# Performance work log

Measured on AMD Instinct MI355X. Metric: run time of the kernel, lower is better.

Reference implementation:

```python
import jax, jax.numpy as jnp
import numpy as np

L = 6        # num_coupling_layers
T_DIM = 64   # t_dim
HALF = T_DIM // 2
COND = 128   # cond_dim
HID = 1024   # hidden_dim
B = 32768


def setup_inputs() -> dict:
    key = jax.random.key(0)
    ks = jax.random.split(key, 8)
    s_in = 1.0 / np.sqrt(HALF + COND)
    s_h = 1.0 / np.sqrt(HID)
    T = jax.random.normal(ks[0], (B, T_DIM), dtype=jnp.float32)
    cond = jax.random.normal(ks[1], (B, COND), dtype=jnp.float32)
    W1 = jax.random.normal(ks[2], (L, HALF + COND, HID), dtype=jnp.float32) * s_in
    b1 = jnp.zeros((L, HID), dtype=jnp.float32)
    W2 = jax.random.normal(ks[3], (L, HID, HID), dtype=jnp.float32) * s_h
    b2 = jnp.zeros((L, HID), dtype=jnp.float32)
    W3 = jax.random.normal(ks[4], (L, HID, 2 * HALF), dtype=jnp.float32) * s_h
    b3 = jnp.zeros((L, 2 * HALF), dtype=jnp.float32)
    return {"T": T, "cond": cond, "W1": W1, "b1": b1, "W2": W2, "b2": b2, "W3": W3, "b3": b3}


def reference(T, cond, W1, b1, W2, b2, W3, b3):
    # Conditional normalizing flow: 6 affine coupling layers with alternating
    # contiguous half masks. Even layers transform the first half, odd the second.
    def mlp(h, i):
        x = jax.nn.relu(h @ W1[i] + b1[i])
        x = jax.nn.relu(x @ W2[i] + b2[i])
        return x @ W3[i] + b3[i]

    z = T
    log_det = jnp.zeros(T.shape[0], dtype=T.dtype)
    for i in range(L):
        if i % 2 == 0:
            masked, unmasked = z[:, :HALF], z[:, HALF:]
        else:
            masked, unmasked = z[:, HALF:], z[:, :HALF]
        params = mlp(jnp.concatenate([unmasked, cond], axis=1), i)
        s = jnp.tanh(params[:, :HALF])
        t_shift = params[:, HALF:]
        y_masked = masked * jnp.exp(s) + t_shift
        if i % 2 == 0:
            z = jnp.concatenate([y_masked, unmasked], axis=1)
        else:
            z = jnp.concatenate([unmasked, y_masked], axis=1)
        log_det = log_det + jnp.sum(s, axis=1)
    return z, log_det
```

## Files before the change

### kernel.cpp

```cpp
#include <hip/hip_runtime.h>
#include <hip/hip_fp16.h>
#include <stdint.h>

typedef _Float16 f16;
typedef _Float16 f16x8 __attribute__((ext_vector_type(8)));
typedef float f32x4 __attribute__((ext_vector_type(4)));

#define NB 32768
#define LAYERS 6
#define AK 160
#define HID 1024

__device__ __forceinline__ void async_copy16(const void* g, void* l) {
  __builtin_amdgcn_global_load_lds(
      (const __attribute__((address_space(1))) void*)g,
      (__attribute__((address_space(3))) void*)l, 16, 0, 0);
}

__device__ __forceinline__ void wtrans_tile(const float* __restrict__ W,
                                            f16* __restrict__ Wt,
                                            const int K_, const int N_,
                                            const int bx, const int by,
                                            const int bz, float (*t)[65])
{
  const long off = (long)bz * K_ * N_;
  const float* Wl = W + off;
  f16* Wtl = Wt + off;
  const int k0 = by * 64, n0 = bx * 64;
  const int tx = threadIdx.x & 63, ty4 = threadIdx.x >> 6;
#pragma unroll
  for (int r = ty4; r < 64; r += 4) {
    const int k = k0 + r;
    if (k < K_) t[r][tx] = Wl[(long)k * N_ + n0 + tx];
  }
  __syncthreads();
  const int k = k0 + tx;
  if (k < K_) {
#pragma unroll
    for (int r = ty4; r < 64; r += 4) {
      const int n = n0 + r;
      Wtl[(long)n * K_ + k] = (f16)t[tx][r];
    }
  }
}

__global__ void prep_all(const float* __restrict__ T, const float* __restrict__ cond,
                         const float* __restrict__ W1, const float* __restrict__ W2,
                         const float* __restrict__ W3,
                         float* __restrict__ z, float* __restrict__ ld,
                         f16* __restrict__ A,
                         f16* __restrict__ W1t, f16* __restrict__ W2t,
                         f16* __restrict__ W3t)
{
  __shared__ float t[64][65];
  const int b = blockIdx.x;
  if (b < 2048) {
    const int S1 = NB * 64;
    const int S2 = S1 + NB;
    const int S3 = S2 + NB * 32;
    const int S4 = S3 + NB * 128;
    for (int i = b * blockDim.x + threadIdx.x; i < S4; i += 2048 * blockDim.x) {
      if (i < S1) {
        z[i] = T[i];
      } else if (i < S2) {
        ld[i - S1] = 0.0f;
      } else if (i < S3) {
        int r = i - S2;
        int row = r >> 5, j = r & 31;
        A[(size_t)row * AK + j] = (f16)T[row * 64 + 32 + j];
      } else {
        int r = i - S3;
        int row = r >> 7, j = r & 127;
        A[(size_t)row * AK + 32 + j] = (f16)cond[r];
      }
    }
  } else if (b < 2048 + 288) {
    const int l = b - 2048;
    wtrans_tile(W1, W1t, AK, 1024, l % 16, (l / 16) % 3, l / 48, t);
  } else if (b < 2048 + 288 + 1536) {
    const int l = b - (2048 + 288);
    wtrans_tile(W2, W2t, HID, 1024, l % 16, (l / 16) % 16, l / 256, t);
  } else {
    const int l = b - (2048 + 288 + 1536);
    wtrans_tile(W3, W3t, HID, 64, 0, l % 16, l / 16, t);
  }
}

__global__ __launch_bounds__(256, 2)
void gemm1_full(const f16* __restrict__ A,
                const f16* __restrict__ Wt,
                const float* __restrict__ bias,
                f16* __restrict__ C)
{
  __shared__ __align__(16) f16 As[128 * 160];
  __shared__ __align__(16) f16 Bs[128 * 160];
  const int tid  = threadIdx.x;
  const int lane = tid & 63;
  const int wave = tid >> 6;
  const int c15  = lane & 15;
  const int quad = lane >> 4;
  const int wm = (wave & 1) * 64;
  const int wn = (wave >> 1) * 64;

  const int b = blockIdx.x;
  const int x = b & 7, i = b >> 3;
  const long rowStart = (long)(x * 32 + (i >> 3)) * 128;
  const long colStart = (long)(i & 7) * 128;

  const f16* Ab = A  + rowStart * AK;
  const f16* Bb = Wt + colStart * AK;

#pragma unroll
  for (int it = 0; it < 10; ++it) {
    const int f = it * 256 + tid;
    const int row = f / 20;
    const int ch  = f - row * 20;
    const int chs = ch ^ ((row >> 1) & 3);
    async_copy16(Ab + (long)row * AK + chs * 8, &As[0] + (long)f * 8);
    async_copy16(Bb + (long)row * AK + chs * 8, &Bs[0] + (long)f * 8);
  }
  __syncthreads();

  f32x4 acc[4][4] = {};
#pragma unroll
  for (int kt = 0; kt < 5; ++kt) {
    f16x8 a[4], bf[4];
#pragma unroll
    for (int mi = 0; mi < 4; ++mi) {
      const int R = wm + mi * 16 + c15;
      a[mi] = *(const f16x8*)&As[(R * 20 + kt * 4 + (quad ^ ((R >> 1) & 3))) * 8];
    }
#pragma unroll
    for (int ni = 0; ni < 4; ++ni) {
      const int R = wn + ni * 16 + c15;
      bf[ni] = *(const f16x8*)&Bs[(R * 20 + kt * 4 + (quad ^ ((R >> 1) & 3))) * 8];
    }
#pragma unroll
    for (int mi = 0; mi < 4; ++mi)
#pragma unroll
      for (int ni = 0; ni < 4; ++ni)
        acc[mi][ni] = __builtin_amdgcn_mfma_f32_16x16x32_f16(
            a[mi], bf[ni], acc[mi][ni], 0, 0, 0);
  }

#pragma unroll
  for (int ni = 0; ni < 4; ++ni) {
    const long gn = colStart + wn + ni * 16 + c15;
    const float bv = bias[gn];
#pragma unroll
    for (int mi = 0; mi < 4; ++mi) {
#pragma unroll
      for (int r = 0; r < 4; ++r) {
        const long gm = rowStart + wm + mi * 16 + quad * 4 + r;
        float v = acc[mi][ni][r] + bv;
        v = fmaxf(v, 0.0f);
        C[gm * HID + gn] = (f16)v;
      }
    }
  }
}

#define RD_A(dst, base, mq) \
  _Pragma("unroll") \
  for (int mi = 0; mi < 4; ++mi) { \
    const int r_ = wm + (mq) * 64 + mi * 16 + c15; \
    _Pragma("unroll") \
    for (int ks = 0; ks < 2; ++ks) \
      dst[mi][ks] = *(const f16x8*)&(base)[r_ * 64 + ((((ks << 2) + quad) ^ (r_ & 7)) << 3)]; \
  }
#define RD_B(dst, base, nq) \
  _Pragma("unroll") \
  for (int ni = 0; ni < 2; ++ni) { \
    const int r_ = wn + (nq) * 32 + ni * 16 + c15; \
    _Pragma("unroll") \
    for (int ks = 0; ks < 2; ++ks) \
      dst[ni][ks] = *(const f16x8*)&(base)[r_ * 64 + ((((ks << 2) + quad) ^ (r_ & 7)) << 3)]; \
  }
#define MM(am, an, afr, bfr) \
  __builtin_amdgcn_s_setprio(1); \
  _Pragma("unroll") \
  for (int ks = 0; ks < 2; ++ks) \
  _Pragma("unroll") \
  for (int mi = 0; mi < 4; ++mi) \
  _Pragma("unroll") \
  for (int ni = 0; ni < 2; ++ni) \
    acc[(am) + mi][(an) + ni] = __builtin_amdgcn_mfma_f32_16x16x32_f16( \
        afr[mi][ks], bfr[ni][ks], acc[(am) + mi][(an) + ni], 0, 0, 0); \
  __builtin_amdgcn_s_setprio(0);
#define BARRIER __builtin_amdgcn_s_barrier()
#define LGKM0   asm volatile("s_waitcnt lgkmcnt(0)")

__global__ __launch_bounds__(512, 2)
void gemm2_8p(const f16* __restrict__ A,
              const f16* __restrict__ Wt,
              const float* __restrict__ bias,
              f16* __restrict__ C)
{
  __shared__ __align__(16) f16 As[2][16384];
  __shared__ __align__(16) f16 Bs[2][16384];

  const int tid  = threadIdx.x;
  const int lane = tid & 63;
  const int wave = tid >> 6;
  const int c15  = lane & 15;
  const int quad = lane >> 4;
  const int wm = (wave >> 2) * 128;
  const int wn = (wave & 3) * 64;

  const int b = blockIdx.x;
  const int wgid = (b & 7) * 64 + (b >> 3);
  const long rowStart = (long)(wgid >> 2) * 256;
  const long colStart = (long)(wgid & 3) * 256;

  const f16* Ab = A  + rowStart * HID;
  const f16* Bb = Wt + colStart * HID;

  const int rh0 = tid >> 3;
  const int ch0 = tid & 7;
  const long g0 = (long)rh0 * HID + ((ch0 ^ (rh0 & 7)) << 3);
  const long g1 = (long)(64 + rh0) * HID + ((ch0 ^ ((64 + rh0) & 7)) << 3);
  const int l0 = tid << 3;
  const int l1 = (512 + tid) << 3;

  auto stA = [&](int kt, int h) {
    const f16* src = Ab + (long)h * 128 * HID + (long)kt * 64;
    f16* dst = &As[kt & 1][h * 8192];
    async_copy16(src + g0, dst + l0);
    async_copy16(src + g1, dst + l1);
  };
  auto stB = [&](int kt, int h) {
    const f16* src = Bb + (long)h * 128 * HID + (long)kt * 64;
    f16* dst = &Bs[kt & 1][h * 8192];
    async_copy16(src + g0, dst + l0);
    async_copy16(src + g1, dst + l1);
  };

  stB(0, 0); stA(0, 0); stB(0, 1); stA(0, 1);
  stB(1, 0); stA(1, 0);
  asm volatile("s_waitcnt vmcnt(4)");
  BARRIER;

  f32x4 acc[8][4] = {};

#pragma unroll 1
  for (int t = 0; t < 8; ++t) {
    const int kt0 = 2 * t, kt1 = 2 * t + 1;
    const f16* asx = &As[0][0];
    const f16* bsx = &Bs[0][0];
    const f16* asy = &As[1][0];
    const f16* bsy = &Bs[1][0];
    const bool pre = (t < 7);
    f16x8 a0[4][2], a1[4][2], b0[2][2], b1[2][2];

    RD_A(a0, asx, 0);
    RD_B(b0, bsx, 0);
    stB(kt1, 1);
    BARRIER; LGKM0;
    MM(0, 0, a0, b0);
    BARRIER;

    RD_B(b1, bsx, 1);
    stA(kt1, 1);
    BARRIER; LGKM0;
    MM(0, 2, a0, b1);
    BARRIER;

    RD_A(a1, asx, 1);
    if (pre) stB(kt0 + 2, 0);
    BARRIER; LGKM0;
    MM(4, 0, a1, b0);
    BARRIER;

    if (pre) stA(kt0 + 2, 0);
    MM(4, 2, a1, b1);
    if (pre) { asm volatile("s_waitcnt vmcnt(4)"); }
    else     { asm volatile("s_waitcnt vmcnt(0)"); }
    BARRIER;

    RD_A(a0, asy, 0);
    RD_B(b0, bsy, 0);
    if (pre) stB(kt0 + 2, 1);
    BARRIER; LGKM0;
    MM(0, 0, a0, b0);
    BARRIER;

    RD_B(b1, bsy, 1);
    if (pre) stA(kt0 + 2, 1);
    BARRIER; LGKM0;
    MM(0, 2, a0, b1);
    BARRIER;

    RD_A(a1, asy, 1);
    if (pre) stB(kt1 + 2, 0);
    BARRIER; LGKM0;
    MM(4, 0, a1, b0);
    BARRIER;

    if (pre) stA(kt1 + 2, 0);
    MM(4, 2, a1, b1);
    if (pre) { asm volatile("s_waitcnt vmcnt(4)"); }
    else     { asm volatile("s_waitcnt vmcnt(0)"); }
    BARRIER;
  }

#pragma unroll
  for (int nii = 0; nii < 4; ++nii) {
    const int nof = (nii >> 1) * 32 + (nii & 1) * 16;
    const long gn = colStart + wn + nof + c15;
    const float bv = bias[gn];
#pragma unroll
    for (int mii = 0; mii < 8; ++mii) {
      const int mof = (mii >> 2) * 64 + (mii & 3) * 16;
#pragma unroll
      for (int r = 0; r < 4; ++r) {
        const long gm = rowStart + wm + mof + quad * 4 + r;
        float v = acc[mii][nii][r] + bv;
        C[gm * HID + gn] = (f16)fmaxf(v, 0.0f);
      }
    }
  }
}

__global__ __launch_bounds__(256, 2)
void gemm3_coupling(const f16* __restrict__ X2, const f16* __restrict__ W3t,
                    const float* __restrict__ b3, float* __restrict__ z,
                    float* __restrict__ log_det, f16* __restrict__ Anext,
                    const int maskoff)
{
  __shared__ __align__(16) f16 As[2][64 * 64];
  __shared__ __align__(16) f16 Bs[2][64 * 64];
  const int tid = threadIdx.x;
  const int wave = tid >> 6, lane = tid & 63;
  const int c15 = lane & 15, quad = lane >> 4;
  const int wm = wave * 16;
  const long rowStart = (long)blockIdx.x * 64;

  const f16* Ab = X2 + rowStart * HID;
  const int brow = tid >> 3;
  const int bkc  = ((tid & 7) ^ (brow & 7)) * 8;

  f32x4 acc[4] = {};

  auto stage = [&](int c, int sel) {
    const long kb = (long)c * 64;
#pragma unroll
    for (int q = 0; q < 2; ++q) {
      async_copy16(Ab  + (long)(q * 32 + brow) * HID + kb + bkc,
                   &As[sel][0] + (q * 256 + wave * 64) * 8);
      async_copy16(W3t + (long)(q * 32 + brow) * HID + kb + bkc,
                   &Bs[sel][0] + (q * 256 + wave * 64) * 8);
    }
  };

  stage(0, 0);
  for (int c = 0; c < 16; ++c) {
    __syncthreads();
    if (c + 1 < 16) stage(c + 1, (c + 1) & 1);
    const f16* as = &As[c & 1][0];
    const f16* bs = &Bs[c & 1][0];

#pragma unroll
    for (int s = 0; s < 2; ++s) {
      const int Ra = wm + c15;
      f16x8 a = *(const f16x8*)&as[(Ra * 8 + ((s * 4 + quad) ^ (Ra & 7))) * 8];
      f16x8 bf[4];
#pragma unroll
      for (int ni = 0; ni < 4; ++ni) {
        const int R = ni * 16 + c15;
        bf[ni] = *(const f16x8*)&bs[(R * 8 + ((s * 4 + quad) ^ (R & 7))) * 8];
      }
#pragma unroll
      for (int ni = 0; ni < 4; ++ni)
        acc[ni] = __builtin_amdgcn_mfma_f32_16x16x32_f16(a, bf[ni], acc[ni], 0, 0, 0);
    }
  }

  float sp[4] = {0.0f, 0.0f, 0.0f, 0.0f};
#pragma unroll
  for (int ni = 0; ni < 2; ++ni) {
    const int j = ni * 16 + c15;
    const float bs = b3[j];
    const float bt = b3[32 + j];
#pragma unroll
    for (int r = 0; r < 4; ++r) {
      const long gm = rowStart + wm + quad * 4 + r;
      const float sv = acc[ni][r] + bs;
      const float e2 = __expf(2.0f * sv);
      const float s  = 1.0f - 2.0f / (e2 + 1.0f);
      const float tv = acc[ni + 2][r] + bt;
      const float m  = z[gm * 64 + maskoff + j];
      const float y  = fmaf(m, __expf(s), tv);
      z[gm * 64 + maskoff + j] = y;
      Anext[gm * AK + j] = (f16)y;
      sp[r] += s;
    }
  }
#pragma unroll
  for (int r = 0; r < 4; ++r) {
    float v = sp[r];
    v += __shfl_xor(v, 1);
    v += __shfl_xor(v, 2);
    v += __shfl_xor(v, 4);
    v += __shfl_xor(v, 8);
    if (c15 == 0) {
      const long gm = rowStart + wm + quad * 4 + r;
      log_det[gm] += v;
    }
  }
}

extern "C" void kernel_launch(void* const* d_in, const int* in_sizes, int n_in,
                              void* d_out, int out_size, void* d_ws, size_t ws_size,
                              hipStream_t stream) {
  (void)in_sizes; (void)n_in; (void)out_size; (void)ws_size;
  const float* T    = (const float*)d_in[0];
  const float* cond = (const float*)d_in[1];
  const float* W1   = (const float*)d_in[2];
  const float* b1   = (const float*)d_in[3];
  const float* W2   = (const float*)d_in[4];
  const float* b2   = (const float*)d_in[5];
  const float* W3   = (const float*)d_in[6];
  const float* b3   = (const float*)d_in[7];

  float* z  = (float*)d_out;
  float* ld = z + (size_t)NB * 64;

  f16* A   = (f16*)d_ws;
  f16* X1  = A   + (size_t)NB * AK;
  f16* X2  = X1  + (size_t)NB * HID;
  f16* W1t = X2  + (size_t)NB * HID;
  f16* W2t = W1t + (size_t)6 * 1024 * 160;
  f16* W3t = W2t + ((size_t)6 << 20);

  prep_all<<<3968, 256, 0, stream>>>(T, cond, W1, W2, W3,
                                     z, ld, A, W1t, W2t, W3t);

  const int g1 = (NB / 128) * (HID / 128);
  const int g2 = (NB / 256) * (HID / 256);
  for (int l = 0; l < LAYERS; ++l) {
    gemm1_full<<<g1, 256, 0, stream>>>(A, W1t + (size_t)l * 1024 * AK,
                                       b1 + l * 1024, X1);
    gemm2_8p<<<g2, 512, 0, stream>>>(X1, W2t + ((size_t)l << 20),
                                     b2 + l * 1024, X2);
    const int maskoff = (l & 1) ? 32 : 0;
    gemm3_coupling<<<NB / 64, 256, 0, stream>>>(X2, W3t + (size_t)l * 64 * 1024,
                                                b3 + l * 64, z, ld, A, maskoff);
  }
}
```

Before: 826.7 us.

## Reschedule gemm2 main loop with register-rotated fragments and partial LDS waits

Rewrites the 1024x1024 hidden GEMM's inner loop so LDS fragment reads for the next MFMA block are issued before the current block runs. It rotates two register fragment sets and waits with partial lgkmcnt counts instead of draining to zero. Global-to-LDS prefetch now loads a whole k-tile up front, issued in pairs per phase, with sched_barrier fencing around vmcnt waits. The aim is to hide LDS latency behind MFMA work, at the cost of more live registers and fragile wait-count correctness.

```diff
diff --git a/kernel.cpp b/kernel.cpp
--- a/kernel.cpp
+++ b/kernel.cpp
@@ -188,10 +188,11 @@
         afr[mi][ks], bfr[ni][ks], acc[(am) + mi][(an) + ni], 0, 0, 0); \
   __builtin_amdgcn_s_setprio(0);
 #define BARRIER __builtin_amdgcn_s_barrier()
-#define LGKM0   asm volatile("s_waitcnt lgkmcnt(0)")
+#define SCHED0  __builtin_amdgcn_sched_barrier(0)
+#define LGKM(n) asm volatile("s_waitcnt lgkmcnt(" #n ")")
 
 __global__ __launch_bounds__(512, 2)
-void gemm2_8p(const f16* __restrict__ A,
+void gemm2_ra(const f16* __restrict__ A,
               const f16* __restrict__ Wt,
               const float* __restrict__ bias,
               f16* __restrict__ C)
@@ -235,71 +236,79 @@
     async_copy16(src + g1, dst + l1);
   };
 
-  stB(0, 0); stA(0, 0); stB(0, 1); stA(0, 1);
-  stB(1, 0); stA(1, 0);
-  asm volatile("s_waitcnt vmcnt(4)");
+  stB(0, 0); stB(0, 1); stA(0, 0); stA(0, 1);
+  stB(1, 0); stB(1, 1); stA(1, 0); stA(1, 1);
+  asm volatile("s_waitcnt vmcnt(8)" ::: "memory");
+  SCHED0;
   BARRIER;
 
   f32x4 acc[8][4] = {};
+  f16x8 aP[4][2], aQ[4][2], bP[2][2], bQ[2][2];
+
+  RD_A(aP, (&As[0][0]), 0);
+  RD_B(bP, (&Bs[0][0]), 0);
 
 #pragma unroll 1
   for (int t = 0; t < 8; ++t) {
     const int kt0 = 2 * t, kt1 = 2 * t + 1;
-    const f16* asx = &As[0][0];
-    const f16* bsx = &Bs[0][0];
-    const f16* asy = &As[1][0];
-    const f16* bsy = &Bs[1][0];
+    const f16* as0 = &As[0][0];
+    const f16* bs0 = &Bs[0][0];
+    const f16* as1 = &As[1][0];
+    const f16* bs1 = &Bs[1][0];
     const bool pre = (t < 7);
-    f16x8 a0[4][2], a1[4][2], b0[2][2], b1[2][2];
-
-    RD_A(a0, asx, 0);
-    RD_B(b0, bsx, 0);
-    stB(kt1, 1);
-    BARRIER; LGKM0;
-    MM(0, 0, a0, b0);
-    BARRIER;
-
-    RD_B(b1, bsx, 1);
-    stA(kt1, 1);
-    BARRIER; LGKM0;
-    MM(0, 2, a0, b1);
-    BARRIER;
-
-    RD_A(a1, asx, 1);
-    if (pre) stB(kt0 + 2, 0);
-    BARRIER; LGKM0;
-    MM(4, 0, a1, b0);
-    BARRIER;
-
-    if (pre) stA(kt0 + 2, 0);
-    MM(4, 2, a1, b1);
-    if (pre) { asm volatile("s_waitcnt vmcnt(4)"); }
-    else     { asm volatile("s_waitcnt vmcnt(0)"); }
-    BARRIER;
-
-    RD_A(a0, asy, 0);
-    RD_B(b0, bsy, 0);
-    if (pre) stB(kt0 + 2, 1);
-    BARRIER; LGKM0;
-    MM(0, 0, a0, b0);
-    BARRIER;
-
-    RD_B(b1, bsy, 1);
-    if (pre) stA(kt0 + 2, 1);
-    BARRIER; LGKM0;
-    MM(0, 2, a0, b1);
-    BARRIER;
-
-    RD_A(a1, asy, 1);
-    if (pre) stB(kt1 + 2, 0);
-    BARRIER; LGKM0;
-    MM(4, 0, a1, b0);
-    BARRIER;
-
-    if (pre) stA(kt1 + 2, 0);
-    MM(4, 2, a1, b1);
-    if (pre) { asm volatile("s_waitcnt vmcnt(4)"); }
-    else     { asm volatile("s_waitcnt vmcnt(0)"); }
+
+    RD_A(aQ, as0, 1);
+    BARRIER;
+    LGKM(8);
+    MM(0, 0, aP, bP);
+    BARRIER;
+
+    RD_B(bQ, bs0, 1);
+    BARRIER;
+    LGKM(4);
+    MM(4, 0, aQ, bP);
+    asm volatile("s_waitcnt vmcnt(0)" ::: "memory");
+    SCHED0;
+    BARRIER;
+
+    RD_B(bP, bs1, 0);
+    if (pre) { stA(kt0 + 2, 0); stA(kt0 + 2, 1); }
+    BARRIER;
+    LGKM(4);
+    MM(4, 2, aQ, bQ);
+    BARRIER;
+
+    RD_A(aQ, as1, 0);
+    if (pre) { stB(kt0 + 2, 0); stB(kt0 + 2, 1); }
+    BARRIER;
+    LGKM(12);
+    MM(0, 2, aP, bQ);
+    BARRIER;
+
+    RD_A(aP, as1, 1);
+    BARRIER;
+    LGKM(8);
+    MM(0, 0, aQ, bP);
+    BARRIER;
+
+    RD_B(bQ, bs1, 1);
+    BARRIER;
+    LGKM(4);
+    MM(4, 0, aP, bP);
+    asm volatile("s_waitcnt vmcnt(0)" ::: "memory");
+    SCHED0;
+    BARRIER;
+
+    if (pre) { RD_B(bP, bs0, 0); stA(kt1 + 2, 0); stA(kt1 + 2, 1); }
+    BARRIER;
+    if (pre) { LGKM(4); } else { LGKM(0); }
+    MM(4, 2, aP, bQ);
+    BARRIER;
+
+    if (pre) { RD_A(aP, as0, 0); stB(kt1 + 2, 0); stB(kt1 + 2, 1); }
+    BARRIER;
+    if (pre) { LGKM(12); } else { LGKM(0); }
+    MM(0, 2, aQ, bQ);
     BARRIER;
   }
 
@@ -440,7 +449,7 @@
   for (int l = 0; l < LAYERS; ++l) {
     gemm1_full<<<g1, 256, 0, stream>>>(A, W1t + (size_t)l * 1024 * AK,
                                        b1 + l * 1024, X1);
-    gemm2_8p<<<g2, 512, 0, stream>>>(X1, W2t + ((size_t)l << 20),
+    gemm2_ra<<<g2, 512, 0, stream>>>(X1, W2t + ((size_t)l << 20),
                                      b2 + l * 1024, X2);
     const int maskoff = (l & 1) ? 32 : 0;
     gemm3_coupling<<<NB / 64, 256, 0, stream>>>(X2, W3t + (size_t)l * 64 * 1024,
```

After: 855.9 us. 1.04x slower.
